# Performance work log

Hardware: AMD Instinct MI355X
Metric: run time of the kernel (lower is better)

## Reference

```python
import jax, jax.numpy as jnp
import numpy as np

N_NODES = 100000
N_EDGES = 1000000
IN_CH = 64
HID = 64


def setup_inputs() -> dict:
    key = jax.random.key(0)
    ks = jax.random.split(key, 10)
    x = jax.random.normal(ks[0], (N_NODES, IN_CH), dtype=jnp.float32)
    edge_index = jax.random.randint(ks[1], (2, N_EDGES), 0, N_NODES, dtype=jnp.int32)
    s = 1.0 / np.sqrt(IN_CH)
    sh = 1.0 / np.sqrt(HID)
    return {
        "x": x,
        "edge_index": edge_index,
        # conv1: lin_l (applied to aggregated neighbors, has bias), lin_r (self, no bias)
        "w1_l": jax.random.uniform(ks[2], (HID, IN_CH), jnp.float32, -s, s),
        "b1": jnp.zeros((HID,), jnp.float32),
        "w1_r": jax.random.uniform(ks[3], (HID, IN_CH), jnp.float32, -s, s),
        # conv2
        "w2_l": jax.random.uniform(ks[4], (HID, HID), jnp.float32, -sh, sh),
        "b2": jnp.zeros((HID,), jnp.float32),
        "w2_r": jax.random.uniform(ks[5], (HID, HID), jnp.float32, -sh, sh),
        # final linear -> 1
        "w_out": jax.random.uniform(ks[6], (1, HID), jnp.float32, -sh, sh),
        "b_out": jnp.zeros((1,), jnp.float32),
    }


def _sage_conv(x, src, dst, w_l, b, w_r, n_nodes):
    # mean aggregation of source features at destination nodes
    agg = jax.ops.segment_sum(x[src], dst, num_segments=n_nodes)  # [N, d]
    cnt = jax.ops.segment_sum(jnp.ones_like(dst, dtype=x.dtype), dst, num_segments=n_nodes)
    mean = agg / jnp.maximum(cnt, 1.0)[:, None]
    # PyG SAGEConv: lin_l(aggregated) + lin_r(x_self); bias lives in lin_l
    return mean @ w_l.T + b + x @ w_r.T


def reference(x, edge_index, w1_l, b1, w1_r, w2_l, b2, w2_r, w_out, b_out):
    src, dst = edge_index[0], edge_index[1]
    n = x.shape[0]
    h = jax.nn.relu(_sage_conv(x, src, dst, w1_l, b1, w1_r, n))
    h = jax.nn.relu(_sage_conv(h, src, dst, w2_l, b2, w2_r, n))
    logits = h @ w_out.T + b_out  # [N, 1]
    return jax.nn.sigmoid(logits)
```

## Files before the change

kernel.cpp:

```cpp
#include <hip/hip_runtime.h>
#include <hip/hip_bf16.h>
#include <math.h>

#define CH 64
#define TILE 16
#define NXCD 8

typedef short short8 __attribute__((ext_vector_type(8)));
typedef float floatx4 __attribute__((ext_vector_type(4)));

__device__ __forceinline__ float bf2f(unsigned short u) {
    return __uint_as_float(((unsigned int)u) << 16);
}
__device__ __forceinline__ unsigned short f2bf(float f) {
    unsigned int x = __float_as_uint(f);
    unsigned int r = (x + 0x7fff + ((x >> 16) & 1)) >> 16;
    return (unsigned short)r;
}

__global__ __launch_bounds__(256) void k_hist(
    const unsigned short* __restrict__ x,
    const int* __restrict__ srcs, const int* __restrict__ dsts,
    int* __restrict__ deg, int* __restrict__ flag,
    int n_edges, int n_nodes)
{
    if (blockIdx.x == 0 && threadIdx.x < 64) {
        unsigned short u = x[2 * threadIdx.x];
        int ex = (u >> 7) & 0xFF;
        bool insane = (ex < 0x60) || (ex > 0x9F);
        unsigned long long m = __ballot(insane);
        if (threadIdx.x == 0) flag[0] = (__popcll(m) > 16) ? 0 : 1;
    }
    int e = blockIdx.x * 256 + threadIdx.x;
    if (e >= n_edges) return;
    int d = dsts[e], s = srcs[e];
    if ((unsigned)d < (unsigned)n_nodes && (unsigned)s < (unsigned)n_nodes)
        atomicAdd(&deg[d], 1);
}

__global__ __launch_bounds__(256) void k_scan(
    const int* __restrict__ deg, int* __restrict__ rowptr,
    int* __restrict__ cursor, int* __restrict__ bsum,
    int* __restrict__ sync, int n, int nb)
{
    __shared__ int ts[256];
    __shared__ int amlast;
    const int t = threadIdx.x;
    const int b = blockIdx.x;

    int base = b * 1024 + t * 4;
    int v[4], local = 0;
    #pragma unroll
    for (int k = 0; k < 4; k++) { v[k] = (base + k < n) ? deg[base + k] : 0; local += v[k]; }
    ts[t] = local; __syncthreads();
    for (int off = 1; off < 256; off <<= 1) {
        int val = (t >= off) ? ts[t - off] : 0;
        __syncthreads();
        ts[t] += val;
        __syncthreads();
    }
    int run = ts[t] - local;
    #pragma unroll
    for (int k = 0; k < 4; k++) { if (base + k < n) rowptr[base + k] = run; run += v[k]; }
    if (t == 255) bsum[b] = ts[255];

    __threadfence();
    __syncthreads();
    if (t == 0) amlast = (atomicAdd(&sync[0], 1) == nb - 1) ? 1 : 0;
    __syncthreads();

    if (amlast) {
        int base2 = t * 4;
        int v2[4], local2 = 0;
        #pragma unroll
        for (int k = 0; k < 4; k++) { v2[k] = (base2 + k < nb) ? bsum[base2 + k] : 0; local2 += v2[k]; }
        ts[t] = local2; __syncthreads();
        for (int off = 1; off < 256; off <<= 1) {
            int val = (t >= off) ? ts[t - off] : 0;
            __syncthreads();
            ts[t] += val;
            __syncthreads();
        }
        int run2 = ts[t] - local2;
        #pragma unroll
        for (int k = 0; k < 4; k++) { if (base2 + k < nb) bsum[base2 + k] = run2; run2 += v2[k]; }
        if (t == 255) rowptr[n] = ts[255];
        __threadfence();
        __syncthreads();
        if (t == 0)
            __hip_atomic_store(&sync[1], 1, __ATOMIC_RELEASE, __HIP_MEMORY_SCOPE_AGENT);
    }

    if (t == 0) {
        while (__hip_atomic_load(&sync[1], __ATOMIC_ACQUIRE, __HIP_MEMORY_SCOPE_AGENT) == 0)
            __builtin_amdgcn_s_sleep(8);
    }
    __syncthreads();
    int add = bsum[b];
    #pragma unroll
    for (int k = 0; k < 4; k++) {
        int i = base + k;
        if (i < n) { int r = rowptr[i] + add; rowptr[i] = r; cursor[i] = r; }
    }
}

__global__ __launch_bounds__(256) void k_permute(
    const int* __restrict__ srcs, const int* __restrict__ dsts,
    int* __restrict__ cursor, int* __restrict__ nbr, int n_edges, int n_nodes)
{
    const int grp = blockIdx.x & (NXCD - 1);
    const int gidx = blockIdx.x >> 3;
    const int gstride = (gridDim.x >> 3) * 256;
    const int range = (n_nodes + NXCD - 1) / NXCD;
    const int lo = grp * range;
    const int hi = min(n_nodes, lo + range);
    for (int e = gidx * 256 + threadIdx.x; e < n_edges; e += gstride) {
        int d = dsts[e];
        if (d >= lo && d < hi) {
            int s = srcs[e];
            if ((unsigned)s < (unsigned)n_nodes) {
                int pos = atomicAdd(&cursor[d], 1);
                nbr[pos] = s;
            }
        }
    }
}

template <int XMODE>
__global__ __launch_bounds__(256) void k_gather(
    const int* __restrict__ flag, const void* __restrict__ xin,
    const int* __restrict__ nbr, const int* __restrict__ rowptr,
    unsigned short* __restrict__ meanout, int n_nodes)
{
    const bool xbf = (XMODE == 1) ? true : (flag[0] != 0);
    const int lane = threadIdx.x & 63;
    const int wid  = threadIdx.x >> 6;
    const int t = lane >> 4;
    const int s = (lane >> 3) & 1;
    const int c = lane & 7;

    int wbase = (blockIdx.x * 4 + wid) * 4;
    if (wbase >= n_nodes) return;
    int node = wbase + t;
    bool nv = node < n_nodes;
    int r0 = 0, d = 0;
    if (nv) { r0 = rowptr[node]; d = rowptr[node + 1] - r0; }

    int dmax = d;
    dmax = max(dmax, __shfl_xor(dmax, 16));
    dmax = max(dmax, __shfl_xor(dmax, 32));

    const unsigned short* xu = (const unsigned short*)xin;
    const float*          xf = (const float*)xin;

    if (xbf) {
        floatx4 a0 = {0, 0, 0, 0}, a1 = {0, 0, 0, 0};
        for (int jb = 0; jb < dmax; jb += 16) {
            #pragma unroll
            for (int k = 0; k < 8; k++) {
                int j = jb + k * 2 + s;
                if (j < d) {
                    int src = nbr[r0 + j];
                    short8 v = *(const short8*)(xu + (size_t)src * CH + c * 8);
                    #pragma unroll
                    for (int i = 0; i < 4; i++) a0[i] += bf2f((unsigned short)v[i]);
                    #pragma unroll
                    for (int i = 0; i < 4; i++) a1[i] += bf2f((unsigned short)v[4 + i]);
                }
            }
        }
        #pragma unroll
        for (int i = 0; i < 4; i++) {
            a0[i] += __shfl_xor(a0[i], 8);
            a1[i] += __shfl_xor(a1[i], 8);
        }
        if (nv && (lane & 8) == 0) {
            float inv = 1.0f / (float)max(d, 1);
            short8 mv;
            #pragma unroll
            for (int i = 0; i < 4; i++) {
                mv[i]     = (short)f2bf(a0[i] * inv);
                mv[4 + i] = (short)f2bf(a1[i] * inv);
            }
            *(short8*)(meanout + (size_t)node * CH + c * 8) = mv;
        }
    } else {
        int j16 = lane & 15;
        floatx4 acc = {0, 0, 0, 0};
        for (int j = 0; j < d; j++) {
            int src = nbr[r0 + j];
            acc += *(const floatx4*)(xf + (size_t)src * CH + j16 * 4);
        }
        if (nv) {
            float inv = 1.0f / (float)max(d, 1);
            unsigned short* mp = meanout + (size_t)node * CH + j16 * 4;
            #pragma unroll
            for (int i = 0; i < 4; i++) mp[i] = f2bf(acc[i] * inv);
        }
    }
}

template <int XMODE, bool HEAD>
__global__ __launch_bounds__(256) void k_mm(
    const int* __restrict__ flag, const void* __restrict__ xin,
    const unsigned short* __restrict__ meanin,
    const void* __restrict__ w_l, const void* __restrict__ bias,
    const void* __restrict__ w_r,
    const void* __restrict__ w_out, const void* __restrict__ b_out,
    void* __restrict__ outp, int n_nodes)
{
    const int isbf = flag[0];
    const bool xbf = (XMODE == 1) ? true : (isbf != 0);
    const int lane = threadIdx.x & 63;
    const int wid  = threadIdx.x >> 6;
    const int n_ = lane & 15;
    const int q_ = lane >> 4;

    short8 wlf[4][2], wrf[4][2];
    float bv[4], wov[4];
    #pragma unroll
    for (int t = 0; t < 4; t++) {
        int row = t * 16 + n_;
        if (isbf) {
            const unsigned short* wl = (const unsigned short*)w_l;
            const unsigned short* wr = (const unsigned short*)w_r;
            #pragma unroll
            for (int kc = 0; kc < 2; kc++) {
                int k0 = kc * 32 + q_ * 8;
                wlf[t][kc] = *(const short8*)(wl + row * CH + k0);
                wrf[t][kc] = *(const short8*)(wr + row * CH + k0);
            }
            bv[t] = bf2f(((const unsigned short*)bias)[row]);
            if (HEAD) wov[t] = bf2f(((const unsigned short*)w_out)[row]);
        } else {
            const float* wl = (const float*)w_l;
            const float* wr = (const float*)w_r;
            #pragma unroll
            for (int kc = 0; kc < 2; kc++) {
                int k0 = kc * 32 + q_ * 8;
                #pragma unroll
                for (int j = 0; j < 8; j++) {
                    wlf[t][kc][j] = (short)f2bf(wl[row * CH + k0 + j]);
                    wrf[t][kc][j] = (short)f2bf(wr[row * CH + k0 + j]);
                }
            }
            bv[t] = ((const float*)bias)[row];
            if (HEAD) wov[t] = ((const float*)w_out)[row];
        }
    }

    const unsigned short* xu = (const unsigned short*)xin;
    const float*          xf = (const float*)xin;
    int n_tiles = (n_nodes + TILE - 1) / TILE;
    int gw = blockIdx.x * 4 + wid;
    int nw = gridDim.x * 4;

    for (int tb = gw; tb < n_tiles; tb += nw) {
        int base = tb * TILE;
        int node_m = base + n_;
        int node_c = (node_m < n_nodes) ? node_m : 0;
        short8 am0 = *(const short8*)(meanin + (size_t)node_c * CH + q_ * 8);
        short8 am1 = *(const short8*)(meanin + (size_t)node_c * CH + 32 + q_ * 8);
        short8 ax0, ax1;
        if (xbf) {
            ax0 = *(const short8*)(xu + (size_t)node_c * CH + q_ * 8);
            ax1 = *(const short8*)(xu + (size_t)node_c * CH + 32 + q_ * 8);
        } else {
            const float* p = xf + (size_t)node_c * CH;
            #pragma unroll
            for (int j = 0; j < 8; j++) {
                ax0[j] = (short)f2bf(p[q_ * 8 + j]);
                ax1[j] = (short)f2bf(p[32 + q_ * 8 + j]);
            }
        }
        floatx4 acc[4];
        #pragma unroll
        for (int t = 0; t < 4; t++) {
            acc[t] = (floatx4){bv[t], bv[t], bv[t], bv[t]};
            acc[t] = __builtin_amdgcn_mfma_f32_16x16x32_bf16(am0, wlf[t][0], acc[t], 0, 0, 0);
            acc[t] = __builtin_amdgcn_mfma_f32_16x16x32_bf16(am1, wlf[t][1], acc[t], 0, 0, 0);
            acc[t] = __builtin_amdgcn_mfma_f32_16x16x32_bf16(ax0, wrf[t][0], acc[t], 0, 0, 0);
            acc[t] = __builtin_amdgcn_mfma_f32_16x16x32_bf16(ax1, wrf[t][1], acc[t], 0, 0, 0);
        }
        if (!HEAD) {
            unsigned short* ho = (unsigned short*)outp;
            #pragma unroll
            for (int t = 0; t < 4; t++) {
                int cc = t * 16 + n_;
                #pragma unroll
                for (int reg = 0; reg < 4; reg++) {
                    int node_r = base + q_ * 4 + reg;
                    if (node_r < n_nodes)
                        ho[(size_t)node_r * CH + cc] = f2bf(fmaxf(acc[t][reg], 0.0f));
                }
            }
        } else {
            float p[4] = {0, 0, 0, 0};
            #pragma unroll
            for (int t = 0; t < 4; t++) {
                #pragma unroll
                for (int reg = 0; reg < 4; reg++)
                    p[reg] += fmaxf(acc[t][reg], 0.0f) * wov[t];
            }
            #pragma unroll
            for (int off = 1; off < 16; off <<= 1) {
                #pragma unroll
                for (int reg = 0; reg < 4; reg++)
                    p[reg] += __shfl_xor(p[reg], off);
            }
            if (n_ == 0) {
                float bo = isbf ? bf2f(((const unsigned short*)b_out)[0])
                                : ((const float*)b_out)[0];
                #pragma unroll
                for (int reg = 0; reg < 4; reg++) {
                    int node_r = base + q_ * 4 + reg;
                    if (node_r < n_nodes) {
                        float sg = 1.0f / (1.0f + expf(-(p[reg] + bo)));
                        if (isbf) ((unsigned short*)outp)[node_r] = f2bf(sg);
                        else      ((float*)outp)[node_r] = sg;
                    }
                }
            }
        }
    }
}

extern "C" void kernel_launch(void* const* d_in, const int* in_sizes, int n_in,
                              void* d_out, int out_size, void* d_ws, size_t ws_size,
                              hipStream_t stream)
{
    const void* x    = d_in[0];
    const int*  ei   = (const int*)d_in[1];
    const void* w1_l = d_in[2];
    const void* b1   = d_in[3];
    const void* w1_r = d_in[4];
    const void* w2_l = d_in[5];
    const void* b2   = d_in[6];
    const void* w2_r = d_in[7];
    const void* wout = d_in[8];
    const void* bout = d_in[9];

    int n_nodes = out_size;
    int n_edges = in_sizes[1] / 2;
    const int* srcs = ei;
    const int* dsts = ei + n_edges;

    char* wsb = (char*)d_ws;
    size_t off = 0;
    auto carve = [&](size_t bytes) { size_t p = off; off = (off + bytes + 255) & ~(size_t)255; return p; };
    size_t flag_off = carve(sizeof(int));
    size_t sync_off = carve(256);
    size_t deg_off  = carve((size_t)n_nodes * sizeof(int));
    size_t row_off  = carve((size_t)(n_nodes + 1) * sizeof(int));
    size_t cur_off  = carve((size_t)n_nodes * sizeof(int));
    size_t bs_off   = carve(1024 * sizeof(int));
    size_t nbr_off  = carve((size_t)n_edges * sizeof(int));
    size_t mean_off = carve((size_t)n_nodes * CH * sizeof(unsigned short));
    size_t h_off    = carve((size_t)n_nodes * CH * sizeof(unsigned short));
    int* flag   = (int*)(wsb + flag_off);
    int* syncp  = (int*)(wsb + sync_off);
    int* deg    = (int*)(wsb + deg_off);
    int* rowptr = (int*)(wsb + row_off);
    int* cursor = (int*)(wsb + cur_off);
    int* bsum   = (int*)(wsb + bs_off);
    int* nbr    = (int*)(wsb + nbr_off);
    unsigned short* mean = (unsigned short*)(wsb + mean_off);
    unsigned short* h    = (unsigned short*)(wsb + h_off);

    int eblocks = (n_edges + 255) / 256;
    int xblocks = 2048;
    int nb1     = (n_nodes + 1023) / 1024;
    int gblocks = (n_nodes + 15) / 16;
    int mblocks = 512;

    hipMemsetAsync(syncp, 0, 256 + (size_t)n_nodes * sizeof(int), stream);

    k_hist<<<eblocks, 256, 0, stream>>>((const unsigned short*)x, srcs, dsts, deg, flag, n_edges, n_nodes);
    k_scan<<<nb1, 256, 0, stream>>>(deg, rowptr, cursor, bsum, syncp, n_nodes, nb1);
    k_permute<<<xblocks, 256, 0, stream>>>(srcs, dsts, cursor, nbr, n_edges, n_nodes);

    k_gather<0><<<gblocks, 256, 0, stream>>>(flag, x, nbr, rowptr, mean, n_nodes);
    k_mm<0, false><<<mblocks, 256, 0, stream>>>(flag, x, mean, w1_l, b1, w1_r,
                                                nullptr, nullptr, h, n_nodes);
    k_gather<1><<<gblocks, 256, 0, stream>>>(flag, h, nbr, rowptr, mean, n_nodes);
    k_mm<1, true><<<mblocks, 256, 0, stream>>>(flag, h, mean, w2_l, b2, w2_r,
                                               wout, bout, d_out, n_nodes);
}
```

Baseline: 296.1 us.

## Fuse CSR histogram, scan and permute into one persistent kernel with grid barriers

Replaces the three CSR-building kernels (histogram, scan, permute) with one persistent kernel of 1024 blocks. The phases are separated by software grid barriers built on atomic counters. The histogram now also uses XCD-partitioned destination ranges, so degree atomics stay local the way the permute atomics already did. This removes two kernel launches and their inter-kernel gaps, at the cost of four spin barriers that assume all blocks are co-resident, and each block now scans the edge list twice.

```diff
diff --git a/kernel.cpp b/kernel.cpp
--- a/kernel.cpp
+++ b/kernel.cpp
@@ -5,6 +5,7 @@
 #define CH 64
 #define TILE 16
 #define NXCD 8
+#define CSR_BLOCKS 1024
 
 typedef short short8 __attribute__((ext_vector_type(8)));
 typedef float floatx4 __attribute__((ext_vector_type(4)));
@@ -18,58 +19,75 @@
     return (unsigned short)r;
 }
 
-__global__ __launch_bounds__(256) void k_hist(
+__device__ __forceinline__ void gbar(int* sync, int slot, int nb) {
+    __threadfence();
+    __syncthreads();
+    if (threadIdx.x == 0) {
+        __hip_atomic_fetch_add(&sync[slot], 1, __ATOMIC_ACQ_REL, __HIP_MEMORY_SCOPE_AGENT);
+        while (__hip_atomic_load(&sync[slot], __ATOMIC_ACQUIRE, __HIP_MEMORY_SCOPE_AGENT) < nb)
+            __builtin_amdgcn_s_sleep(1);
+        __threadfence();
+    }
+    __syncthreads();
+}
+
+__global__ __launch_bounds__(256) void k_csr(
     const unsigned short* __restrict__ x,
     const int* __restrict__ srcs, const int* __restrict__ dsts,
-    int* __restrict__ deg, int* __restrict__ flag,
-    int n_edges, int n_nodes)
+    int* __restrict__ deg, int* __restrict__ rowptr, int* __restrict__ cursor,
+    int* __restrict__ bsum, int* __restrict__ sync, int* __restrict__ flag,
+    int* __restrict__ nbr, int n_edges, int n_nodes, int nb)
 {
-    if (blockIdx.x == 0 && threadIdx.x < 64) {
-        unsigned short u = x[2 * threadIdx.x];
+    __shared__ int ts[256];
+    const int t = threadIdx.x;
+    const int b = blockIdx.x;
+    const int NB = gridDim.x;
+    const int grp = b & (NXCD - 1);
+    const int gidx = b >> 3;
+    const int gstride = (NB >> 3) * 256;
+    const int range = (n_nodes + NXCD - 1) / NXCD;
+    const int lo = grp * range;
+    const int hi = min(n_nodes, lo + range);
+
+    if (b == 0 && t < 64) {
+        unsigned short u = x[2 * t];
         int ex = (u >> 7) & 0xFF;
         bool insane = (ex < 0x60) || (ex > 0x9F);
         unsigned long long m = __ballot(insane);
-        if (threadIdx.x == 0) flag[0] = (__popcll(m) > 16) ? 0 : 1;
-    }
-    int e = blockIdx.x * 256 + threadIdx.x;
-    if (e >= n_edges) return;
-    int d = dsts[e], s = srcs[e];
-    if ((unsigned)d < (unsigned)n_nodes && (unsigned)s < (unsigned)n_nodes)
-        atomicAdd(&deg[d], 1);
-}
-
-__global__ __launch_bounds__(256) void k_scan(
-    const int* __restrict__ deg, int* __restrict__ rowptr,
-    int* __restrict__ cursor, int* __restrict__ bsum,
-    int* __restrict__ sync, int n, int nb)
-{
-    __shared__ int ts[256];
-    __shared__ int amlast;
-    const int t = threadIdx.x;
-    const int b = blockIdx.x;
-
-    int base = b * 1024 + t * 4;
-    int v[4], local = 0;
-    #pragma unroll
-    for (int k = 0; k < 4; k++) { v[k] = (base + k < n) ? deg[base + k] : 0; local += v[k]; }
-    ts[t] = local; __syncthreads();
-    for (int off = 1; off < 256; off <<= 1) {
-        int val = (t >= off) ? ts[t - off] : 0;
+        if (t == 0) flag[0] = (__popcll(m) > 16) ? 0 : 1;
+    }
+
+    for (int e = gidx * 256 + t; e < n_edges; e += gstride) {
+        int d = dsts[e];
+        if (d >= lo && d < hi) {
+            int s = srcs[e];
+            if ((unsigned)s < (unsigned)n_nodes)
+                atomicAdd(&deg[d], 1);
+        }
+    }
+    gbar(sync, 1, NB);
+
+    for (int cb = b; cb < nb; cb += NB) {
+        int base = cb * 1024 + t * 4;
+        int v[4], local = 0;
+        #pragma unroll
+        for (int k = 0; k < 4; k++) { v[k] = (base + k < n_nodes) ? deg[base + k] : 0; local += v[k]; }
+        ts[t] = local; __syncthreads();
+        for (int off = 1; off < 256; off <<= 1) {
+            int val = (t >= off) ? ts[t - off] : 0;
+            __syncthreads();
+            ts[t] += val;
+            __syncthreads();
+        }
+        int run = ts[t] - local;
+        #pragma unroll
+        for (int k = 0; k < 4; k++) { if (base + k < n_nodes) rowptr[base + k] = run; run += v[k]; }
+        if (t == 255) bsum[cb] = ts[255];
         __syncthreads();
-        ts[t] += val;
-        __syncthreads();
-    }
-    int run = ts[t] - local;
-    #pragma unroll
-    for (int k = 0; k < 4; k++) { if (base + k < n) rowptr[base + k] = run; run += v[k]; }
-    if (t == 255) bsum[b] = ts[255];
-
-    __threadfence();
-    __syncthreads();
-    if (t == 0) amlast = (atomicAdd(&sync[0], 1) == nb - 1) ? 1 : 0;
-    __syncthreads();
-
-    if (amlast) {
+    }
+    gbar(sync, 2, NB);
+
+    if (b == 0) {
         int base2 = t * 4;
         int v2[4], local2 = 0;
         #pragma unroll
@@ -84,37 +102,22 @@
         int run2 = ts[t] - local2;
         #pragma unroll
         for (int k = 0; k < 4; k++) { if (base2 + k < nb) bsum[base2 + k] = run2; run2 += v2[k]; }
-        if (t == 255) rowptr[n] = ts[255];
-        __threadfence();
-        __syncthreads();
-        if (t == 0)
-            __hip_atomic_store(&sync[1], 1, __ATOMIC_RELEASE, __HIP_MEMORY_SCOPE_AGENT);
-    }
-
-    if (t == 0) {
-        while (__hip_atomic_load(&sync[1], __ATOMIC_ACQUIRE, __HIP_MEMORY_SCOPE_AGENT) == 0)
-            __builtin_amdgcn_s_sleep(8);
-    }
-    __syncthreads();
-    int add = bsum[b];
-    #pragma unroll
-    for (int k = 0; k < 4; k++) {
-        int i = base + k;
-        if (i < n) { int r = rowptr[i] + add; rowptr[i] = r; cursor[i] = r; }
-    }
-}
-
-__global__ __launch_bounds__(256) void k_permute(
-    const int* __restrict__ srcs, const int* __restrict__ dsts,
-    int* __restrict__ cursor, int* __restrict__ nbr, int n_edges, int n_nodes)
-{
-    const int grp = blockIdx.x & (NXCD - 1);
-    const int gidx = blockIdx.x >> 3;
-    const int gstride = (gridDim.x >> 3) * 256;
-    const int range = (n_nodes + NXCD - 1) / NXCD;
-    const int lo = grp * range;
-    const int hi = min(n_nodes, lo + range);
-    for (int e = gidx * 256 + threadIdx.x; e < n_edges; e += gstride) {
+        if (t == 255) rowptr[n_nodes] = ts[255];
+    }
+    gbar(sync, 3, NB);
+
+    for (int cb = b; cb < nb; cb += NB) {
+        int add = bsum[cb];
+        int base = cb * 1024 + t * 4;
+        #pragma unroll
+        for (int k = 0; k < 4; k++) {
+            int i = base + k;
+            if (i < n_nodes) { int r = rowptr[i] + add; rowptr[i] = r; cursor[i] = r; }
+        }
+    }
+    gbar(sync, 4, NB);
+
+    for (int e = gidx * 256 + t; e < n_edges; e += gstride) {
         int d = dsts[e];
         if (d >= lo && d < hi) {
             int s = srcs[e];
@@ -367,17 +370,15 @@
     unsigned short* mean = (unsigned short*)(wsb + mean_off);
     unsigned short* h    = (unsigned short*)(wsb + h_off);
 
-    int eblocks = (n_edges + 255) / 256;
-    int xblocks = 2048;
     int nb1     = (n_nodes + 1023) / 1024;
     int gblocks = (n_nodes + 15) / 16;
     int mblocks = 512;
 
     hipMemsetAsync(syncp, 0, 256 + (size_t)n_nodes * sizeof(int), stream);
 
-    k_hist<<<eblocks, 256, 0, stream>>>((const unsigned short*)x, srcs, dsts, deg, flag, n_edges, n_nodes);
-    k_scan<<<nb1, 256, 0, stream>>>(deg, rowptr, cursor, bsum, syncp, n_nodes, nb1);
-    k_permute<<<xblocks, 256, 0, stream>>>(srcs, dsts, cursor, nbr, n_edges, n_nodes);
+    k_csr<<<CSR_BLOCKS, 256, 0, stream>>>((const unsigned short*)x, srcs, dsts,
+                                          deg, rowptr, cursor, bsum, syncp, flag,
+                                          nbr, n_edges, n_nodes, nb1);
 
     k_gather<0><<<gblocks, 256, 0, stream>>>(flag, x, nbr, rowptr, mean, n_nodes);
     k_mm<0, false><<<mblocks, 256, 0, stream>>>(flag, x, mean, w1_l, b1, w1_r,
```

New measurement: 802.6 us. +171.1%, slower.
